# Kernel tuning notes

Hardware: AMD Instinct MI355X
Metric: run time of the kernel (lower is better)

Reference implementation:

```python
import jax, jax.numpy as jnp
import numpy as np
import math

E = 8          # num_experts
IN = 1024      # input_size
HID = 512      # head_size (expert hidden)
TOP_K = 2
B, P = 8, 1024


def setup_inputs() -> dict:
    key = jax.random.key(0)
    k1, k2, k3, k4, k5 = jax.random.split(key, 5)
    # expert weights init like ParallelExperts.reset_parameters (uniform xavier-ish)
    std1 = math.sqrt(2.0 / (IN + HID)); a1 = math.sqrt(3.0) * std1
    std2 = math.sqrt(2.0 / (HID + IN)); a2 = math.sqrt(3.0) * std2
    return {
        "x": jax.random.normal(k1, (B, P, IN), dtype=jnp.float32),
        "Q_isp": jax.random.normal(k2, (B, P, 1, IN), dtype=jnp.float32),
        "K_isp": jax.random.normal(k3, (B, P, E, IN), dtype=jnp.float32),
        "w1": jax.random.uniform(k4, (E, IN, HID), minval=-a1, maxval=a1, dtype=jnp.float32),
        "w2": jax.random.uniform(k5, (E, HID, IN), minval=-a2, maxval=a2, dtype=jnp.float32),
    }


def _gates(Q_isp, K_isp):
    # attention-based gating, eval path (no noise)
    N = K_isp.shape[2]
    scale = 1.0 / math.sqrt(K_isp.shape[-1])
    # [B,P,1,N] -> [T,N]
    scores = jnp.einsum('bpqd,bpnd->bpqn', Q_isp, K_isp)[:, :, 0, :].reshape(-1, N) * scale
    logits = jnp.nan_to_num(scores, nan=0.0, posinf=20.0, neginf=-20.0)
    probs = jax.nn.softmax(logits, axis=1)
    top_g, top_i = jax.lax.top_k(probs, TOP_K)
    # renormalize top-k gates; denominator detached as in torch (.detach())
    top_g = top_g / jax.lax.stop_gradient(top_g.sum(axis=1, keepdims=True) + 1e-6)
    T = probs.shape[0]
    gates = jnp.zeros_like(probs).at[jnp.arange(T)[:, None], top_i].set(top_g)
    return gates  # [T, E]


def reference(x, Q_isp, K_isp, w1, w2):
    gates = _gates(Q_isp, K_isp)                       # [T,E]
    T = gates.shape[0]
    xt = x.reshape(T, -1)                              # [T,IN]
    # grouped expert GEMMs (dense-masked form; gates are 0 off top-k)
    h = jax.nn.gelu(jnp.einsum('ti,eio->teo', xt, w1), approximate=False)  # [T,E,HID]
    y = jnp.einsum('teo,eoi->tei', h, w2)              # [T,E,IN]
    out = jnp.einsum('tei,te->ti', y, gates)           # combine with gates
    return out.reshape(x.shape)
```

## Files before the change

kernel.cpp:

```cpp
#include <hip/hip_runtime.h>
#include <math.h>

#define TT 8192
#define NE 8
#define DIN 1024
#define DH 512
#define MT_MAX 136

typedef __attribute__((ext_vector_type(8))) short short8;
typedef __attribute__((ext_vector_type(4))) float f32x4;
typedef __attribute__((ext_vector_type(4))) unsigned short us4;

static const size_t OFF_BASE   = 0;
static const size_t OFF_TOKEXP = 256;
static const size_t OFF_GPAIR  = OFF_TOKEXP + (size_t)TT * 8;
static const size_t OFF_TOK    = OFF_GPAIR  + (size_t)TT * 8;
static const size_t OFF_GATE   = OFF_TOK    + (size_t)(2 * TT + NE * 128) * 4;
static const size_t OFF_XB     = OFF_GATE   + (size_t)(2 * TT + NE * 128) * 4;
static const size_t OFF_W1T    = OFF_XB     + (size_t)TT * DIN * 2;
static const size_t OFF_W2T    = OFF_W1T    + (size_t)NE * DH * DIN * 2;
static const size_t OFF_H      = OFF_W2T    + (size_t)NE * DIN * DH * 2;

__device__ __forceinline__ unsigned short f2bf(float f) {
    union { float f; unsigned u; } v; v.f = f;
    unsigned r = (v.u + 0x7fffu + ((v.u >> 16) & 1u)) >> 16;
    return (unsigned short)r;
}
__device__ __forceinline__ void async_copy16(const void* g, void* l) {
    __builtin_amdgcn_global_load_lds(
        (const __attribute__((address_space(1))) void*)g,
        (__attribute__((address_space(3))) void*)l, 16, 0, 0);
}

__device__ __forceinline__ float gelu_erf(float u) {
    float z  = 0.70710678118f * u;
    float az = fabsf(z);
    float t  = __builtin_amdgcn_rcpf(__builtin_fmaf(0.3275911f, az, 1.0f));
    float p  = t * (0.254829592f + t * (-0.284496736f + t * (1.421413741f +
               t * (-1.453152027f + t * 1.061405429f))));
    float e2 = exp2f(-1.4426950408889634f * az * az);
    float er = __builtin_fmaf(-p, e2, 1.0f);
    er = copysignf(er, z);
    return 0.5f * u * (1.0f + er);
}

__global__ __launch_bounds__(256) void prep_kernel(
    const float* __restrict__ x, const float* __restrict__ w1, const float* __restrict__ w2,
    const float* __restrict__ Q, const float* __restrict__ Kc,
    unsigned short* __restrict__ xb, unsigned short* __restrict__ w1t,
    unsigned short* __restrict__ w2t,
    int2* __restrict__ tokexp, float2* __restrict__ gpair,
    float* __restrict__ out)
{
    __shared__ float tile[32][33];
    int bid = blockIdx.x;
    int tid = threadIdx.x;

    if (bid < 2048) {
        int wave = tid >> 6, lane = tid & 63;
        int t = bid * 4 + wave;
        const float4* q4 = reinterpret_cast<const float4*>(Q + (size_t)t * DIN);
        const float4* k4 = reinterpret_cast<const float4*>(Kc + (size_t)t * NE * DIN);
        float4 q[4];
#pragma unroll
        for (int j = 0; j < 4; ++j) q[j] = q4[j * 64 + lane];
        float part[NE];
#pragma unroll
        for (int e = 0; e < NE; ++e) {
            float s = 0.0f;
#pragma unroll
            for (int j = 0; j < 4; ++j) {
                float4 kv = k4[e * 256 + j * 64 + lane];
                s += q[j].x * kv.x + q[j].y * kv.y + q[j].z * kv.z + q[j].w * kv.w;
            }
            part[e] = s;
        }
#pragma unroll
        for (int e = 0; e < NE; ++e) {
#pragma unroll
            for (int m = 1; m < 64; m <<= 1) part[e] += __shfl_xor(part[e], m);
        }
        if (lane == 0) {
            float s[NE];
#pragma unroll
            for (int e = 0; e < NE; ++e) {
                float v = part[e] * 0.03125f;
                if (isnan(v)) v = 0.0f;
                else if (isinf(v)) v = (v > 0.0f) ? 20.0f : -20.0f;
                s[e] = v;
            }
            float m = s[0];
            for (int e = 1; e < NE; ++e) m = fmaxf(m, s[e]);
            float p[NE]; float sum = 0.0f;
            for (int e = 0; e < NE; ++e) { p[e] = expf(s[e] - m); sum += p[e]; }
            float inv = 1.0f / sum;
            for (int e = 0; e < NE; ++e) p[e] *= inv;
            int i0 = 0;
            for (int e = 1; e < NE; ++e) if (p[e] > p[i0]) i0 = e;
            int i1 = (i0 == 0) ? 1 : 0;
            for (int e = 0; e < NE; ++e) if (e != i0 && p[e] > p[i1]) i1 = e;
            float denom = p[i0] + p[i1] + 1e-6f;
            tokexp[t] = make_int2(i0, i1);
            gpair[t]  = make_float2(p[i0] / denom, p[i1] / denom);
        }
    } else if (bid < 4096) {
        size_t i = ((size_t)(bid - 2048) * 256 + tid) * 16;
        float4 z = {0.f, 0.f, 0.f, 0.f};
#pragma unroll
        for (int j = 0; j < 4; ++j)
            *reinterpret_cast<float4*>(out + i + j * 4) = z;
    } else if (bid < 8192) {
        size_t i = ((size_t)(bid - 4096) * 256 + tid) * 8;
        float4 a = *reinterpret_cast<const float4*>(x + i);
        float4 b = *reinterpret_cast<const float4*>(x + i + 4);
        us4 o0 = { f2bf(a.x), f2bf(a.y), f2bf(a.z), f2bf(a.w) };
        us4 o1 = { f2bf(b.x), f2bf(b.y), f2bf(b.z), f2bf(b.w) };
        *reinterpret_cast<us4*>(xb + i)     = o0;
        *reinterpret_cast<us4*>(xb + i + 4) = o1;
    } else {
        const float* src; unsigned short* dst; int K, N, e, k0, n0;
        if (bid < 12288) {
            int r = bid - 8192; e = r >> 9; int rem = r & 511;
            k0 = (rem & 31) * 32; n0 = (rem >> 5) * 32;
            src = w1; dst = w1t; K = DIN; N = DH;
        } else {
            int r = bid - 12288; e = r >> 9; int rem = r & 511;
            k0 = (rem & 15) * 32; n0 = (rem >> 4) * 32;
            src = w2; dst = w2t; K = DH; N = DIN;
        }
        int tx = tid & 31, ty = tid >> 5;
        const float* s = src + ((size_t)e * K + k0) * N + n0;
#pragma unroll
        for (int r2 = 0; r2 < 32; r2 += 8) tile[ty + r2][tx] = s[(size_t)(ty + r2) * N + tx];
        __syncthreads();
        unsigned short* d = dst + ((size_t)e * N + n0) * K + k0;
#pragma unroll
        for (int r2 = 0; r2 < 32; r2 += 8) d[(size_t)(ty + r2) * K + tx] = f2bf(tile[tx][ty + r2]);
    }
}

__global__ __launch_bounds__(1024) void route_kernel(
    const int2* __restrict__ tokexp, const float2* __restrict__ gpair,
    int* __restrict__ base,
    int* __restrict__ tok_list, float* __restrict__ gate_list)
{
    int e = blockIdx.x;
    int tid = threadIdx.x;
    int wave = tid >> 6, lane = tid & 63;
    __shared__ int hist[NE];
    __shared__ int wsum[16];
    __shared__ int running;

    if (tid < NE) hist[tid] = 0;
    __syncthreads();

    int lc[NE];
#pragma unroll
    for (int j = 0; j < NE; ++j) lc[j] = 0;
#pragma unroll
    for (int r = 0; r < TT / 1024; ++r) {
        int2 te = tokexp[r * 1024 + tid];
#pragma unroll
        for (int j = 0; j < NE; ++j) lc[j] += (te.x == j ? 1 : 0) + (te.y == j ? 1 : 0);
    }
#pragma unroll
    for (int j = 0; j < NE; ++j) {
        int v = lc[j];
#pragma unroll
        for (int m = 1; m < 64; m <<= 1) v += __shfl_xor(v, m);
        if (lane == 0) atomicAdd(&hist[j], v);
    }
    __syncthreads();

    int basep[NE + 1];
    basep[0] = 0;
#pragma unroll
    for (int j = 0; j < NE; ++j) basep[j + 1] = basep[j] + ((hist[j] + 127) & ~127);

    if (tid == 0) {
        base[e] = basep[e];
        if (e == 0) base[NE] = basep[NE];
        running = basep[e];
    }
    __syncthreads();

    int myb = basep[e];
    int cnt_e = hist[e];
#pragma unroll 1
    for (int r = 0; r < TT / 1024; ++r) {
        int t = r * 1024 + tid;
        int2 te = tokexp[t];
        float2 g = gpair[t];
        bool f0 = (te.x == e), f1 = (te.y == e);
        bool f = f0 || f1;
        unsigned long long mask = __ballot(f);
        int mypos = __popcll(mask & ((1ull << lane) - 1ull));
        if (lane == 0) wsum[wave] = __popcll(mask);
        __syncthreads();
        int off = 0, total = 0;
        for (int w = 0; w < 16; ++w) {
            int c = wsum[w];
            if (w < wave) off += c;
            total += c;
        }
        int pos = running + off + mypos;
        if (f) {
            tok_list[pos]  = t;
            gate_list[pos] = f0 ? g.x : g.y;
        }
        __syncthreads();
        if (tid == 0) running += total;
        __syncthreads();
    }

    int padn = ((cnt_e + 127) & ~127) - cnt_e;
    if (tid < padn) {
        tok_list[myb + cnt_e + tid]  = 0;
        gate_list[myb + cnt_e + tid] = 0.0f;
    }
}

__global__ __launch_bounds__(256) void gemm1_kernel(
    const unsigned short* __restrict__ xb, const unsigned short* __restrict__ w1t,
    const int* __restrict__ base,
    const int* __restrict__ tok_list, unsigned short* __restrict__ h)
{
    int bv[NE + 1];
#pragma unroll
    for (int i = 0; i <= NE; ++i) bv[i] = base[i];
    int g0 = blockIdx.x * 128;
    if (g0 >= bv[NE]) return;
    int e = 0;
#pragma unroll
    for (int i = 1; i < NE; ++i) if (g0 >= bv[i]) e = i;

    int n0 = blockIdx.y * 128;

    __shared__ __align__(16) char smem[65536];

    int tid = threadIdx.x;
    int w = tid >> 6, lane = tid & 63;
    int wm = w & 1, wn = w >> 1;
    int mcol = lane & 15;
    int kq = (lane >> 4) * 8;

    int ra0 = tok_list[g0 + (2 * w + 0) * 16 + mcol];
    int ra1 = tok_list[g0 + (2 * w + 1) * 16 + mcol];

    const unsigned short* w1e = w1t + (size_t)e * DH * DIN;
    const unsigned short* pa0 = xb + (size_t)ra0 * DIN + kq;
    const unsigned short* pa1 = xb + (size_t)ra1 * DIN + kq;
    const unsigned short* pb0 = w1e + (size_t)(n0 + (2 * w + 0) * 16 + mcol) * DIN + kq;
    const unsigned short* pb1 = w1e + (size_t)(n0 + (2 * w + 1) * 16 + mcol) * DIN + kq;

    int d0 = (2 * w + 0) * 1024;
    int d1 = (2 * w + 1) * 1024;

#define STAGE1(buf, koff) do { \
    async_copy16(pa0 + (koff),      (buf) + d0); \
    async_copy16(pa1 + (koff),      (buf) + d1); \
    async_copy16(pa0 + (koff) + 32, (buf) + 8192  + d0); \
    async_copy16(pa1 + (koff) + 32, (buf) + 8192  + d1); \
    async_copy16(pb0 + (koff),      (buf) + 16384 + d0); \
    async_copy16(pb1 + (koff),      (buf) + 16384 + d1); \
    async_copy16(pb0 + (koff) + 32, (buf) + 24576 + d0); \
    async_copy16(pb1 + (koff) + 32, (buf) + 24576 + d1); \
} while (0)

    f32x4 acc[4][4];
#pragma unroll
    for (int i = 0; i < 4; i++)
#pragma unroll
        for (int j = 0; j < 4; j++) acc[i][j] = {0.f, 0.f, 0.f, 0.f};

    char* cur = smem;
    char* nxt = smem + 32768;

    STAGE1(cur, 0);
    __syncthreads();

    const int NT = DIN / 64;
    for (int t = 0; t < NT; ++t) {
        if (t + 1 < NT) STAGE1(nxt, (t + 1) * 64);
#pragma unroll
        for (int half = 0; half < 2; ++half) {
            const char* cb = cur + half * 8192;
            short8 af[4], bfr[4];
#pragma unroll
            for (int mt = 0; mt < 4; ++mt)
                af[mt] = *reinterpret_cast<const short8*>(cb + (wm * 4 + mt) * 1024 + lane * 16);
#pragma unroll
            for (int nt = 0; nt < 4; ++nt)
                bfr[nt] = *reinterpret_cast<const short8*>(cb + 16384 + (wn * 4 + nt) * 1024 + lane * 16);
#pragma unroll
            for (int mt = 0; mt < 4; ++mt)
#pragma unroll
                for (int nt = 0; nt < 4; ++nt)
                    acc[mt][nt] = __builtin_amdgcn_mfma_f32_16x16x32_bf16(af[mt], bfr[nt], acc[mt][nt], 0, 0, 0);
        }
        __syncthreads();
        char* tmp = cur; cur = nxt; nxt = tmp;
    }
#undef STAGE1

#pragma unroll
    for (int mt = 0; mt < 4; ++mt) {
        int rbase = (wm * 4 + mt) * 16 + ((lane >> 4) * 4);
#pragma unroll
        for (int r = 0; r < 4; ++r) {
            int row = rbase + r;
#pragma unroll
            for (int nt = 0; nt < 4; ++nt) {
                float g = gelu_erf(acc[mt][nt][r]);
                int col = n0 + (wn * 4 + nt) * 16 + mcol;
                h[(size_t)(g0 + row) * DH + col] = f2bf(g);
            }
        }
    }
}

__global__ __launch_bounds__(256) void gemm2_kernel(
    const unsigned short* __restrict__ h, const unsigned short* __restrict__ w2t,
    const int* __restrict__ base,
    const int* __restrict__ tok_list, const float* __restrict__ gate_list,
    float* __restrict__ out)
{
    int bv[NE + 1];
#pragma unroll
    for (int i = 0; i <= NE; ++i) bv[i] = base[i];
    int g0 = blockIdx.x * 128;
    if (g0 >= bv[NE]) return;
    int e = 0;
#pragma unroll
    for (int i = 1; i < NE; ++i) if (g0 >= bv[i]) e = i;

    int n0 = blockIdx.y * 128;

    __shared__ __align__(16) char smem[65536];

    int tid = threadIdx.x;
    int w = tid >> 6, lane = tid & 63;
    int wm = w & 1, wn = w >> 1;
    int mcol = lane & 15;
    int kq = (lane >> 4) * 8;

    const unsigned short* w2e = w2t + (size_t)e * DIN * DH;
    const unsigned short* pa0 = h + (size_t)(g0 + (2 * w + 0) * 16 + mcol) * DH + kq;
    const unsigned short* pa1 = h + (size_t)(g0 + (2 * w + 1) * 16 + mcol) * DH + kq;
    const unsigned short* pb0 = w2e + (size_t)(n0 + (2 * w + 0) * 16 + mcol) * DH + kq;
    const unsigned short* pb1 = w2e + (size_t)(n0 + (2 * w + 1) * 16 + mcol) * DH + kq;

    int d0 = (2 * w + 0) * 1024;
    int d1 = (2 * w + 1) * 1024;

#define STAGE2(buf, koff) do { \
    async_copy16(pa0 + (koff),      (buf) + d0); \
    async_copy16(pa1 + (koff),      (buf) + d1); \
    async_copy16(pa0 + (koff) + 32, (buf) + 8192  + d0); \
    async_copy16(pa1 + (koff) + 32, (buf) + 8192  + d1); \
    async_copy16(pb0 + (koff),      (buf) + 16384 + d0); \
    async_copy16(pb1 + (koff),      (buf) + 16384 + d1); \
    async_copy16(pb0 + (koff) + 32, (buf) + 24576 + d0); \
    async_copy16(pb1 + (koff) + 32, (buf) + 24576 + d1); \
} while (0)

    f32x4 acc[4][4];
#pragma unroll
    for (int i = 0; i < 4; i++)
#pragma unroll
        for (int j = 0; j < 4; j++) acc[i][j] = {0.f, 0.f, 0.f, 0.f};

    char* cur = smem;
    char* nxt = smem + 32768;

    STAGE2(cur, 0);
    __syncthreads();

    const int NT = DH / 64;
    for (int t = 0; t < NT; ++t) {
        if (t + 1 < NT) STAGE2(nxt, (t + 1) * 64);
#pragma unroll
        for (int half = 0; half < 2; ++half) {
            const char* cb = cur + half * 8192;
            short8 af[4], bfr[4];
#pragma unroll
            for (int mt = 0; mt < 4; ++mt)
                af[mt] = *reinterpret_cast<const short8*>(cb + (wm * 4 + mt) * 1024 + lane * 16);
#pragma unroll
            for (int nt = 0; nt < 4; ++nt)
                bfr[nt] = *reinterpret_cast<const short8*>(cb + 16384 + (wn * 4 + nt) * 1024 + lane * 16);
#pragma unroll
            for (int mt = 0; mt < 4; ++mt)
#pragma unroll
                for (int nt = 0; nt < 4; ++nt)
                    acc[mt][nt] = __builtin_amdgcn_mfma_f32_16x16x32_bf16(af[mt], bfr[nt], acc[mt][nt], 0, 0, 0);
        }
        __syncthreads();
        char* tmp = cur; cur = nxt; nxt = tmp;
    }
#undef STAGE2

#pragma unroll
    for (int mt = 0; mt < 4; ++mt) {
        int rbase = (wm * 4 + mt) * 16 + ((lane >> 4) * 4);
#pragma unroll
        for (int r = 0; r < 4; ++r) {
            int row = rbase + r;
            int tok = tok_list[g0 + row];
            float g = gate_list[g0 + row];
#pragma unroll
            for (int nt = 0; nt < 4; ++nt) {
                int col = n0 + (wn * 4 + nt) * 16 + mcol;
                atomicAdd(&out[(size_t)tok * DIN + col], acc[mt][nt][r] * g);
            }
        }
    }
}

extern "C" void kernel_launch(void* const* d_in, const int* in_sizes, int n_in,
                              void* d_out, int out_size, void* d_ws, size_t ws_size,
                              hipStream_t stream) {
    const float* x  = (const float*)d_in[0];
    const float* Q  = (const float*)d_in[1];
    const float* K  = (const float*)d_in[2];
    const float* w1 = (const float*)d_in[3];
    const float* w2 = (const float*)d_in[4];
    float* out = (float*)d_out;

    char* ws = (char*)d_ws;
    int*    base      = (int*)(ws + OFF_BASE);
    int2*   tokexp    = (int2*)(ws + OFF_TOKEXP);
    float2* gpair     = (float2*)(ws + OFF_GPAIR);
    int*    tok_list  = (int*)(ws + OFF_TOK);
    float*  gate_list = (float*)(ws + OFF_GATE);
    unsigned short* xb  = (unsigned short*)(ws + OFF_XB);
    unsigned short* w1t = (unsigned short*)(ws + OFF_W1T);
    unsigned short* w2t = (unsigned short*)(ws + OFF_W2T);
    unsigned short* h   = (unsigned short*)(ws + OFF_H);

    prep_kernel<<<16384, 256, 0, stream>>>(x, w1, w2, Q, K, xb, w1t, w2t, tokexp, gpair, out);
    route_kernel<<<NE, 1024, 0, stream>>>(tokexp, gpair, base, tok_list, gate_list);
    gemm1_kernel<<<dim3(MT_MAX, DH / 128), 256, 0, stream>>>(xb, w1t, base, tok_list, h);
    gemm2_kernel<<<dim3(MT_MAX, DIN / 128), 256, 0, stream>>>(h, w2t, base, tok_list, gate_list, out);
}
```

Before: 655.7 us.

## Replace atomic scatter-add with bf16 per-slot output and gather combine kernel

gemm2 now writes gated results as bf16 into a per-slot buffer y instead of doing atomicAdd into the fp32 output. A new combine kernel gathers each token's two slots through slot indices recorded by the router and writes the sum. This removes the zeroing of out and the contended atomics. In exchange it adds an extra kernel launch, a 16MB-scale intermediate write and read, and bf16 rounding of the per-expert partial outputs.

```diff
diff --git a/kernel.cpp b/kernel.cpp
--- a/kernel.cpp
+++ b/kernel.cpp
@@ -11,20 +11,28 @@
 typedef __attribute__((ext_vector_type(4))) float f32x4;
 typedef __attribute__((ext_vector_type(4))) unsigned short us4;
 
+static const size_t NSLOT      = (size_t)(2 * TT + NE * 128);
 static const size_t OFF_BASE   = 0;
 static const size_t OFF_TOKEXP = 256;
 static const size_t OFF_GPAIR  = OFF_TOKEXP + (size_t)TT * 8;
-static const size_t OFF_TOK    = OFF_GPAIR  + (size_t)TT * 8;
-static const size_t OFF_GATE   = OFF_TOK    + (size_t)(2 * TT + NE * 128) * 4;
-static const size_t OFF_XB     = OFF_GATE   + (size_t)(2 * TT + NE * 128) * 4;
+static const size_t OFF_SLOT0  = OFF_GPAIR  + (size_t)TT * 8;
+static const size_t OFF_SLOT1  = OFF_SLOT0  + (size_t)TT * 4;
+static const size_t OFF_TOK    = OFF_SLOT1  + (size_t)TT * 4;
+static const size_t OFF_GATE   = OFF_TOK    + NSLOT * 4;
+static const size_t OFF_XB     = OFF_GATE   + NSLOT * 4;
 static const size_t OFF_W1T    = OFF_XB     + (size_t)TT * DIN * 2;
 static const size_t OFF_W2T    = OFF_W1T    + (size_t)NE * DH * DIN * 2;
 static const size_t OFF_H      = OFF_W2T    + (size_t)NE * DIN * DH * 2;
+static const size_t OFF_Y      = OFF_H      + NSLOT * DH * 2;
 
 __device__ __forceinline__ unsigned short f2bf(float f) {
     union { float f; unsigned u; } v; v.f = f;
     unsigned r = (v.u + 0x7fffu + ((v.u >> 16) & 1u)) >> 16;
     return (unsigned short)r;
+}
+__device__ __forceinline__ float bf2f(unsigned short u) {
+    union { unsigned u; float f; } v; v.u = ((unsigned)u) << 16;
+    return v.f;
 }
 __device__ __forceinline__ void async_copy16(const void* g, void* l) {
     __builtin_amdgcn_global_load_lds(
@@ -49,8 +57,7 @@
     const float* __restrict__ Q, const float* __restrict__ Kc,
     unsigned short* __restrict__ xb, unsigned short* __restrict__ w1t,
     unsigned short* __restrict__ w2t,
-    int2* __restrict__ tokexp, float2* __restrict__ gpair,
-    float* __restrict__ out)
+    int2* __restrict__ tokexp, float2* __restrict__ gpair)
 {
     __shared__ float tile[32][33];
     int bid = blockIdx.x;
@@ -103,14 +110,8 @@
             tokexp[t] = make_int2(i0, i1);
             gpair[t]  = make_float2(p[i0] / denom, p[i1] / denom);
         }
-    } else if (bid < 4096) {
-        size_t i = ((size_t)(bid - 2048) * 256 + tid) * 16;
-        float4 z = {0.f, 0.f, 0.f, 0.f};
-#pragma unroll
-        for (int j = 0; j < 4; ++j)
-            *reinterpret_cast<float4*>(out + i + j * 4) = z;
-    } else if (bid < 8192) {
-        size_t i = ((size_t)(bid - 4096) * 256 + tid) * 8;
+    } else if (bid < 6144) {
+        size_t i = ((size_t)(bid - 2048) * 256 + tid) * 8;
         float4 a = *reinterpret_cast<const float4*>(x + i);
         float4 b = *reinterpret_cast<const float4*>(x + i + 4);
         us4 o0 = { f2bf(a.x), f2bf(a.y), f2bf(a.z), f2bf(a.w) };
@@ -119,12 +120,12 @@
         *reinterpret_cast<us4*>(xb + i + 4) = o1;
     } else {
         const float* src; unsigned short* dst; int K, N, e, k0, n0;
-        if (bid < 12288) {
-            int r = bid - 8192; e = r >> 9; int rem = r & 511;
+        if (bid < 10240) {
+            int r = bid - 6144; e = r >> 9; int rem = r & 511;
             k0 = (rem & 31) * 32; n0 = (rem >> 5) * 32;
             src = w1; dst = w1t; K = DIN; N = DH;
         } else {
-            int r = bid - 12288; e = r >> 9; int rem = r & 511;
+            int r = bid - 10240; e = r >> 9; int rem = r & 511;
             k0 = (rem & 15) * 32; n0 = (rem >> 4) * 32;
             src = w2; dst = w2t; K = DH; N = DIN;
         }
@@ -142,7 +143,8 @@
 __global__ __launch_bounds__(1024) void route_kernel(
     const int2* __restrict__ tokexp, const float2* __restrict__ gpair,
     int* __restrict__ base,
-    int* __restrict__ tok_list, float* __restrict__ gate_list)
+    int* __restrict__ tok_list, float* __restrict__ gate_list,
+    int* __restrict__ slot0, int* __restrict__ slot1)
 {
     int e = blockIdx.x;
     int tid = threadIdx.x;
@@ -207,6 +209,7 @@
         if (f) {
             tok_list[pos]  = t;
             gate_list[pos] = f0 ? g.x : g.y;
+            if (f0) slot0[t] = pos; else slot1[t] = pos;
         }
         __syncthreads();
         if (tid == 0) running += total;
@@ -322,8 +325,7 @@
 __global__ __launch_bounds__(256) void gemm2_kernel(
     const unsigned short* __restrict__ h, const unsigned short* __restrict__ w2t,
     const int* __restrict__ base,
-    const int* __restrict__ tok_list, const float* __restrict__ gate_list,
-    float* __restrict__ out)
+    const float* __restrict__ gate_list, unsigned short* __restrict__ y)
 {
     int bv[NE + 1];
 #pragma unroll
@@ -406,14 +408,35 @@
 #pragma unroll
         for (int r = 0; r < 4; ++r) {
             int row = rbase + r;
-            int tok = tok_list[g0 + row];
             float g = gate_list[g0 + row];
 #pragma unroll
             for (int nt = 0; nt < 4; ++nt) {
                 int col = n0 + (wn * 4 + nt) * 16 + mcol;
-                atomicAdd(&out[(size_t)tok * DIN + col], acc[mt][nt][r] * g);
+                y[(size_t)(g0 + row) * DIN + col] = f2bf(acc[mt][nt][r] * g);
             }
         }
+    }
+}
+
+__global__ __launch_bounds__(256) void combine_kernel(
+    const unsigned short* __restrict__ y,
+    const int* __restrict__ slot0, const int* __restrict__ slot1,
+    float* __restrict__ out)
+{
+    int c = threadIdx.x * 4;
+#pragma unroll
+    for (int r = 0; r < 4; ++r) {
+        int t = blockIdx.x * 4 + r;
+        const unsigned short* y0 = y + (size_t)slot0[t] * DIN + c;
+        const unsigned short* y1 = y + (size_t)slot1[t] * DIN + c;
+        us4 u0 = *reinterpret_cast<const us4*>(y0);
+        us4 u1 = *reinterpret_cast<const us4*>(y1);
+        float4 o;
+        o.x = bf2f(u0.x) + bf2f(u1.x);
+        o.y = bf2f(u0.y) + bf2f(u1.y);
+        o.z = bf2f(u0.z) + bf2f(u1.z);
+        o.w = bf2f(u0.w) + bf2f(u1.w);
+        *reinterpret_cast<float4*>(out + (size_t)t * DIN + c) = o;
     }
 }
 
@@ -431,15 +454,19 @@
     int*    base      = (int*)(ws + OFF_BASE);
     int2*   tokexp    = (int2*)(ws + OFF_TOKEXP);
     float2* gpair     = (float2*)(ws + OFF_GPAIR);
+    int*    slot0     = (int*)(ws + OFF_SLOT0);
+    int*    slot1     = (int*)(ws + OFF_SLOT1);
     int*    tok_list  = (int*)(ws + OFF_TOK);
     float*  gate_list = (float*)(ws + OFF_GATE);
     unsigned short* xb  = (unsigned short*)(ws + OFF_XB);
     unsigned short* w1t = (unsigned short*)(ws + OFF_W1T);
     unsigned short* w2t = (unsigned short*)(ws + OFF_W2T);
     unsigned short* h   = (unsigned short*)(ws + OFF_H);
-
-    prep_kernel<<<16384, 256, 0, stream>>>(x, w1, w2, Q, K, xb, w1t, w2t, tokexp, gpair, out);
-    route_kernel<<<NE, 1024, 0, stream>>>(tokexp, gpair, base, tok_list, gate_list);
+    unsigned short* y   = (unsigned short*)(ws + OFF_Y);
+
+    prep_kernel<<<14336, 256, 0, stream>>>(x, w1, w2, Q, K, xb, w1t, w2t, tokexp, gpair);
+    route_kernel<<<NE, 1024, 0, stream>>>(tokexp, gpair, base, tok_list, gate_list, slot0, slot1);
     gemm1_kernel<<<dim3(MT_MAX, DH / 128), 256, 0, stream>>>(xb, w1t, base, tok_list, h);
-    gemm2_kernel<<<dim3(MT_MAX, DIN / 128), 256, 0, stream>>>(h, w2t, base, tok_list, gate_list, out);
-}
+    gemm2_kernel<<<dim3(MT_MAX, DIN / 128), 256, 0, stream>>>(h, w2t, base, gate_list, y);
+    combine_kernel<<<TT / 4, 256, 0, stream>>>(y, slot0, slot1, out);
+}
```

After: 551.5 us. 1.19x faster.
